# Optimization experiments

Measured on AMD Instinct MI355X. Metric: run time of the kernel, lower is better.

Reference implementation:

```python
import jax, jax.numpy as jnp
import numpy as np

B, T, C, H = 8, 1024, 1024, 16
Dh = C // H
EPS = 1e-5


def layernorm(x, g, b):
    m = jnp.mean(x, axis=-1, keepdims=True)
    v = jnp.mean((x - m) ** 2, axis=-1, keepdims=True)
    return g * (x - m) / jnp.sqrt(v + EPS) + b


def setup_inputs() -> dict:
    key = jax.random.key(0)
    ks = jax.random.split(key, 10)
    s = 0.02
    return {
        "x": jax.random.normal(ks[0], (B, T, C), jnp.float32),
        "Wq": jax.random.normal(ks[1], (H, C, Dh), jnp.float32) * s,
        "Wk": jax.random.normal(ks[2], (H, C, Dh), jnp.float32) * s,
        "Wv": jax.random.normal(ks[3], (H, C, Dh), jnp.float32) * s,
        "Wproj": jax.random.normal(ks[4], (C, C), jnp.float32) * s,
        "bproj": jnp.zeros((C,), jnp.float32),
        "W1": jax.random.normal(ks[5], (C, C), jnp.float32) * s,
        "b1": jnp.zeros((C,), jnp.float32),
        "W2": jax.random.normal(ks[6], (C, C), jnp.float32) * s,
        "b2": jnp.zeros((C,), jnp.float32),
        "g1": jnp.ones((C,), jnp.float32),
        "beta1": jnp.zeros((C,), jnp.float32),
        "g2": jnp.ones((C,), jnp.float32),
        "beta2": jnp.zeros((C,), jnp.float32),
    }


def reference(x, Wq, Wk, Wv, Wproj, bproj, W1, b1, W2, b2, g1, beta1, g2, beta2):
    # pre-LN multi-head causal self-attention + residual
    xn = layernorm(x, g1, beta1)
    q = jnp.einsum("btc,hcd->bhtd", xn, Wq)
    k = jnp.einsum("btc,hcd->bhtd", xn, Wk)
    v = jnp.einsum("btc,hcd->bhtd", xn, Wv)
    scores = jnp.einsum("bhtd,bhsd->bhts", q, k) * (Dh ** -0.5)
    causal = jnp.tril(jnp.ones((T, T), bool))  # [T,T]
    scores = jnp.where(causal, scores, -jnp.inf)
    wei = jax.nn.softmax(scores, axis=-1)
    attn = jnp.einsum("bhts,bhsd->bhtd", wei, v)
    attn = attn.transpose(0, 2, 1, 3).reshape(B, T, C)  # concat heads
    x = x + attn @ Wproj + bproj
    # pre-LN MLP (n_emb -> n_emb, ReLU, n_emb -> n_emb) + residual
    xn2 = layernorm(x, g2, beta2)
    h = jax.nn.relu(xn2 @ W1 + b1)
    x = x + h @ W2 + b2
    return x
```

## Files before the change

kernel.cpp:

```cpp
#include <hip/hip_runtime.h>
#include <hip/hip_bf16.h>

#define KDIM 1024

typedef __bf16  bf16x8  __attribute__((ext_vector_type(8)));
typedef float   floatx4 __attribute__((ext_vector_type(4)));

__device__ inline short f2bf(float f) {
    unsigned u = __float_as_uint(f);
    u += 0x7fffu + ((u >> 16) & 1u);
    return (short)(u >> 16);
}
__device__ inline float bf2f(short s) {
    return __uint_as_float(((unsigned)(unsigned short)s) << 16);
}

__device__ inline floatx4 mfma16(bf16x8 a, bf16x8 b, floatx4 c) {
    return __builtin_amdgcn_mfma_f32_16x16x32_bf16(a, b, c, 0, 0, 0);
}

__device__ inline void load_lds16(const void* g, void* l) {
    __builtin_amdgcn_global_load_lds(
        (__attribute__((address_space(1))) void*)(unsigned long long)g,
        (__attribute__((address_space(3))) void*)(unsigned)(unsigned long long)l,
        16, 0, 0);
}

template <bool BF16IN>
__global__ __launch_bounds__(256) void ln_kernel(
    const void* __restrict__ xv, const float* __restrict__ g,
    const float* __restrict__ be, short* __restrict__ out)
{
    const int row = blockIdx.x, tid = threadIdx.x;
    float4 v;
    if constexpr (BF16IN) {
        const short4 s4 = ((const short4*)xv)[(size_t)row * 256 + tid];
        v.x = bf2f(s4.x); v.y = bf2f(s4.y); v.z = bf2f(s4.z); v.w = bf2f(s4.w);
    } else {
        v = ((const float4*)xv)[(size_t)row * 256 + tid];
    }
    float s  = v.x + v.y + v.z + v.w;
    float s2 = v.x * v.x + v.y * v.y + v.z * v.z + v.w * v.w;
    #pragma unroll
    for (int off = 32; off; off >>= 1) {
        s  += __shfl_down(s, off);
        s2 += __shfl_down(s2, off);
    }
    __shared__ float red1[4], red2[4];
    const int w = tid >> 6, lane = tid & 63;
    if (lane == 0) { red1[w] = s; red2[w] = s2; }
    __syncthreads();
    s  = red1[0] + red1[1] + red1[2] + red1[3];
    s2 = red2[0] + red2[1] + red2[2] + red2[3];
    const float mean = s * (1.0f / 1024.0f);
    const float var  = s2 * (1.0f / 1024.0f) - mean * mean;
    const float rstd = rsqrtf(var + 1e-5f);
    const float4 gg = ((const float4*)g)[tid];
    const float4 bb = ((const float4*)be)[tid];
    short4 o;
    o.x = f2bf((v.x - mean) * rstd * gg.x + bb.x);
    o.y = f2bf((v.y - mean) * rstd * gg.y + bb.y);
    o.z = f2bf((v.z - mean) * rstd * gg.z + bb.z);
    o.w = f2bf((v.w - mean) * rstd * gg.w + bb.w);
    *(short4*)(out + (size_t)row * 1024 + tid * 4) = o;
}

__global__ void pack_all(const float* __restrict__ Wq, const float* __restrict__ Wk,
                         const float* __restrict__ Wv, const float* __restrict__ Wproj,
                         const float* __restrict__ W1, const float* __restrict__ W2,
                         short* __restrict__ qkvT, short* __restrict__ projT,
                         short* __restrict__ w1T, short* __restrict__ w2T)
{
    __shared__ float tile[32][33];
    const int bx = blockIdx.x, c0 = blockIdx.y * 32;
    const int tx = threadIdx.x, ty = threadIdx.y;
    if (bx < 96) {
        const int n0 = bx * 32;
        const int grp = n0 >> 10;
        const float* W = (grp == 0) ? Wq : (grp == 1 ? Wk : Wv);
        const int nb = n0 & 1023, hh = nb >> 6, d0 = nb & 63;
        #pragma unroll
        for (int j = 0; j < 32; j += 8)
            tile[ty + j][tx] = W[hh * 65536 + (c0 + ty + j) * 64 + d0 + tx];
        __syncthreads();
        #pragma unroll
        for (int j = 0; j < 32; j += 8)
            qkvT[(size_t)(n0 + ty + j) * 1024 + c0 + tx] = f2bf(tile[tx][ty + j]);
    } else {
        const int which = (bx - 96) >> 5;
        const int n0 = ((bx - 96) & 31) * 32;
        const float* src = (which == 0) ? Wproj : (which == 1 ? W1 : W2);
        short* dst = (which == 0) ? projT : (which == 1 ? w1T : w2T);
        #pragma unroll
        for (int j = 0; j < 32; j += 8)
            tile[ty + j][tx] = src[(size_t)(c0 + ty + j) * 1024 + n0 + tx];
        __syncthreads();
        #pragma unroll
        for (int j = 0; j < 32; j += 8)
            dst[(size_t)(n0 + ty + j) * 1024 + c0 + tx] = f2bf(tile[tx][ty + j]);
    }
}

template <int EPI, bool SWAP, int TM>
__global__ __launch_bounds__(256, 4) void gemm_bt(
    const short* __restrict__ A, const short* __restrict__ BT, int N,
    const float* __restrict__ bias, const float* __restrict__ residF,
    const short* __restrict__ residH,
    float* __restrict__ outF, short* __restrict__ outH,
    short* __restrict__ qO, short* __restrict__ kO, short* __restrict__ vtO)
{
    constexpr int IT = TM / 32;
    constexpr int PP = (8192 / TM) / 8;
    const int tid = threadIdx.x, lane = tid & 63, w = tid >> 6;
    const int wm = w >> 1, wn = w & 1;
    const int mi = lane & 15, quad = lane >> 4;
    const int lid = blockIdx.x + gridDim.x * blockIdx.y;
    const int xcd = lid & 7, i8 = lid >> 3;
    const int rowBase = (xcd * PP + (i8 % PP)) * TM;
    const int colBase = (i8 / PP) * 128;

    __shared__ alignas(16) short As[2][TM * 32];
    __shared__ alignas(16) short Bs[2][128 * 32];

    const floatx4 z4 = {0.f, 0.f, 0.f, 0.f};
    floatx4 acc[IT][4];
    #pragma unroll
    for (int i = 0; i < IT; ++i)
        #pragma unroll
        for (int j = 0; j < 4; ++j) acc[i][j] = z4;

    auto stage = [&](int k0, int buf) {
        #pragma unroll
        for (int i = 0; i < TM / 64; ++i) {
            const int cb = i * 256 + w * 64;
            const int chunk = cb + lane;
            const int r = chunk >> 2, cc = chunk & 3;
            const int csw = cc ^ ((r >> 1) & 3);
            load_lds16(A + (size_t)(rowBase + r) * KDIM + k0 + csw * 8,
                       (char*)As[buf] + cb * 16);
        }
        #pragma unroll
        for (int i = 0; i < 2; ++i) {
            const int cb = i * 256 + w * 64;
            const int chunk = cb + lane;
            const int r = chunk >> 2, cc = chunk & 3;
            const int csw = cc ^ ((r >> 1) & 3);
            load_lds16(BT + (size_t)(colBase + r) * KDIM + k0 + csw * 8,
                       (char*)Bs[buf] + cb * 16);
        }
    };

    auto compute = [&](const short* Ac, const short* Bc) {
        bf16x8 af[IT], bfv[4];
        #pragma unroll
        for (int it = 0; it < IT; ++it) {
            const int ra = wm * (TM / 2) + it * 16 + mi;
            af[it] = *(const bf16x8*)(Ac + ra * 32 + ((quad ^ ((ra >> 1) & 3)) << 3));
        }
        #pragma unroll
        for (int jt = 0; jt < 4; ++jt) {
            const int rb = wn * 64 + jt * 16 + mi;
            bfv[jt] = *(const bf16x8*)(Bc + rb * 32 + ((quad ^ ((rb >> 1) & 3)) << 3));
        }
        #pragma unroll
        for (int it = 0; it < IT; ++it)
            #pragma unroll
            for (int jt = 0; jt < 4; ++jt) {
                if constexpr (SWAP)
                    acc[it][jt] = mfma16(bfv[jt], af[it], acc[it][jt]);
                else
                    acc[it][jt] = mfma16(af[it], bfv[jt], acc[it][jt]);
            }
    };

    stage(0, 0);
    #pragma unroll 1
    for (int c = 0; c < KDIM / 32; c += 2) {
        __syncthreads();
        if (c + 1 < KDIM / 32) stage((c + 1) * 32, 1);
        compute(As[0], Bs[0]);
        __syncthreads();
        if (c + 2 < KDIM / 32) stage((c + 2) * 32, 0);
        compute(As[1], Bs[1]);
    }

    if constexpr (SWAP) {
        #pragma unroll
        for (int it = 0; it < IT; ++it) {
            const int row = rowBase + wm * (TM / 2) + it * 16 + mi;
            #pragma unroll
            for (int jt = 0; jt < 4; ++jt) {
                const int col0 = colBase + wn * 64 + jt * 16 + quad * 4;
                const floatx4 a4 = acc[it][jt];
                if constexpr (EPI == 0) {
                    if (colBase < 1024) {
                        short4 o;
                        o.x = f2bf(a4[0] * 0.125f); o.y = f2bf(a4[1] * 0.125f);
                        o.z = f2bf(a4[2] * 0.125f); o.w = f2bf(a4[3] * 0.125f);
                        *(short4*)(qO + (size_t)row * 1024 + col0) = o;
                    } else {
                        short4 o;
                        o.x = f2bf(a4[0]); o.y = f2bf(a4[1]);
                        o.z = f2bf(a4[2]); o.w = f2bf(a4[3]);
                        *(short4*)(kO + (size_t)row * 1024 + (col0 - 1024)) = o;
                    }
                } else if constexpr (EPI == 2) {
                    const float4 b4 = *(const float4*)(bias + col0);
                    short4 o;
                    o.x = f2bf(fmaxf(a4[0] + b4.x, 0.f));
                    o.y = f2bf(fmaxf(a4[1] + b4.y, 0.f));
                    o.z = f2bf(fmaxf(a4[2] + b4.z, 0.f));
                    o.w = f2bf(fmaxf(a4[3] + b4.w, 0.f));
                    *(short4*)(outH + (size_t)row * N + col0) = o;
                } else if constexpr (EPI == 4) {
                    const float4 b4 = *(const float4*)(bias + col0);
                    const float4 r4 = *(const float4*)(residF + (size_t)row * N + col0);
                    short4 o;
                    o.x = f2bf(a4[0] + b4.x + r4.x);
                    o.y = f2bf(a4[1] + b4.y + r4.y);
                    o.z = f2bf(a4[2] + b4.z + r4.z);
                    o.w = f2bf(a4[3] + b4.w + r4.w);
                    *(short4*)(outH + (size_t)row * N + col0) = o;
                } else {
                    const float4 b4 = *(const float4*)(bias + col0);
                    const short4 r4 = *(const short4*)(residH + (size_t)row * N + col0);
                    float4 o;
                    o.x = a4[0] + b4.x + bf2f(r4.x);
                    o.y = a4[1] + b4.y + bf2f(r4.y);
                    o.z = a4[2] + b4.z + bf2f(r4.z);
                    o.w = a4[3] + b4.w + bf2f(r4.w);
                    *(float4*)(outF + (size_t)row * N + col0) = o;
                }
            }
        }
    } else {
        #pragma unroll
        for (int it = 0; it < IT; ++it) {
            const int row0 = rowBase + wm * (TM / 2) + it * 16 + quad * 4;
            const int bb = row0 >> 10, t0 = row0 & 1023;
            #pragma unroll
            for (int jt = 0; jt < 4; ++jt) {
                const int c = colBase + wn * 64 + jt * 16 + mi;
                const floatx4 a4 = acc[it][jt];
                short4 o;
                o.x = f2bf(a4[0]); o.y = f2bf(a4[1]);
                o.z = f2bf(a4[2]); o.w = f2bf(a4[3]);
                *(short4*)(vtO + ((size_t)bb << 20) + ((size_t)c << 10) + t0) = o;
            }
        }
    }
}

#define PSTR 88
__device__ __forceinline__ void attn_qk_pv(
    const bf16x8 qf0, const bf16x8 qf1,
    floatx4 (&o)[4], float (&lsum)[4],
    const short* Ks, const short* Vs, short* myP,
    const int mi, const int quad, const int kq, const int diagRowOff)
{
    const floatx4 z4 = {0.f, 0.f, 0.f, 0.f};
    const bool diag = diagRowOff >= 0;
    floatx4 sa[4];
    #pragma unroll
    for (int j = 0; j < 4; ++j) {
        const int row = j * 16 + mi;
        const int sw = row & 7;
        floatx4 s4 = z4;
        s4 = mfma16(qf0, *(const bf16x8*)(Ks + row * 64 + ((quad ^ sw) << 3)), s4);
        s4 = mfma16(qf1, *(const bf16x8*)(Ks + row * 64 + (((quad + 4) ^ sw) << 3)), s4);
        sa[j] = s4;
    }
    #pragma unroll
    for (int j = 0; j < 4; ++j)
        #pragma unroll
        for (int r = 0; r < 4; ++r) {
            float p = __expf(sa[j][r]);
            if (diag && (j * 16 + mi > diagRowOff + quad * 4 + r)) p = 0.f;
            lsum[r] += p;
            myP[(quad * 4 + r) * PSTR + j * 16 + mi] = f2bf(p);
        }
    __asm__ volatile("s_waitcnt lgkmcnt(0)" ::: "memory");
    const bf16x8 pf0 = *(const bf16x8*)(myP + mi * PSTR + kq);
    const bf16x8 pf1 = *(const bf16x8*)(myP + mi * PSTR + 32 + kq);
    #pragma unroll
    for (int d = 0; d < 4; ++d) {
        const int row = d * 16 + mi;
        const int sw = row & 7;
        o[d] = mfma16(pf0, *(const bf16x8*)(Vs + row * 64 + ((quad ^ sw) << 3)), o[d]);
        o[d] = mfma16(pf1, *(const bf16x8*)(Vs + row * 64 + (((quad + 4) ^ sw) << 3)), o[d]);
    }
}

__global__ __launch_bounds__(256, 4) void flash_attn(
    const short* __restrict__ Q, const short* __restrict__ K,
    const short* __restrict__ Vt, short* __restrict__ O)
{
    const int tid = threadIdx.x, lane = tid & 63, w = tid >> 6;
    const int mi = lane & 15, quad = lane >> 4, kq = quad * 8;
    const int lid = blockIdx.x;
    const int xcd = lid & 7, i8 = lid >> 3;
    const int bh = xcd * 16 + (i8 & 15);
    const int pi = i8 >> 4;
    const int h = bh & 15, b = bh >> 4;
    const int tA = pi, tB = 15 - pi;
    const int qbA = tA * 64, qbB = tB * 64;

    __shared__ alignas(16) short Ks[64 * 64];
    __shared__ alignas(16) short Vs[64 * 64];
    __shared__ alignas(16) short Ps[4][16 * PSTR];

    const size_t qoffA = ((size_t)(b * 1024 + qbA + w * 16 + mi)) * 1024 + h * 64;
    const size_t qoffB = ((size_t)(b * 1024 + qbB + w * 16 + mi)) * 1024 + h * 64;
    const bf16x8 qA0 = *(const bf16x8*)(Q + qoffA + kq);
    const bf16x8 qA1 = *(const bf16x8*)(Q + qoffA + 32 + kq);
    const bf16x8 qB0 = *(const bf16x8*)(Q + qoffB + kq);
    const bf16x8 qB1 = *(const bf16x8*)(Q + qoffB + 32 + kq);

    const floatx4 z4 = {0.f, 0.f, 0.f, 0.f};
    floatx4 oA[4], oB[4];
    float lA[4], lB[4];
    #pragma unroll
    for (int i = 0; i < 4; ++i) { oA[i] = z4; oB[i] = z4; lA[i] = 0.f; lB[i] = 0.f; }

    short* myP = &Ps[w][0];
    for (int t = 0; t <= tB; ++t) {
        const int s0 = t * 64;
        __syncthreads();
        #pragma unroll
        for (int i = 0; i < 2; ++i) {
            const int cb = i * 256 + w * 64;
            const int chunk = cb + lane;
            const int r = chunk >> 3, c = chunk & 7;
            const int csw = c ^ (r & 7);
            load_lds16(K + ((size_t)(b * 1024 + s0 + r)) * 1024 + h * 64 + csw * 8,
                       (char*)Ks + cb * 16);
            load_lds16(Vt + ((size_t)b << 20) + ((size_t)(h * 64 + r) << 10) + s0 + csw * 8,
                       (char*)Vs + cb * 16);
        }
        __syncthreads();

        if (t <= tA)
            attn_qk_pv(qA0, qA1, oA, lA, Ks, Vs, myP, mi, quad, kq,
                       (t == tA) ? (w * 16) : -1);
        attn_qk_pv(qB0, qB1, oB, lB, Ks, Vs, myP, mi, quad, kq,
                   (t == tB) ? (w * 16) : -1);
    }

    #pragma unroll
    for (int r = 0; r < 4; ++r) {
        float sA = lA[r], sB = lB[r];
        #pragma unroll
        for (int off = 1; off < 16; off <<= 1) {
            sA += __shfl_xor(sA, off);
            sB += __shfl_xor(sB, off);
        }
        lA[r] = 1.0f / sA;
        lB[r] = 1.0f / sB;
    }
    #pragma unroll
    for (int d = 0; d < 4; ++d)
        #pragma unroll
        for (int r = 0; r < 4; ++r) {
            const int col = h * 64 + d * 16 + mi;
            const int rowA = b * 1024 + qbA + w * 16 + quad * 4 + r;
            const int rowB = b * 1024 + qbB + w * 16 + quad * 4 + r;
            O[(size_t)rowA * 1024 + col] = f2bf(oA[d][r] * lA[r]);
            O[(size_t)rowB * 1024 + col] = f2bf(oB[d][r] * lB[r]);
        }
}

extern "C" void kernel_launch(void* const* d_in, const int* in_sizes, int n_in,
                              void* d_out, int out_size, void* d_ws, size_t ws_size,
                              hipStream_t stream)
{
    (void)in_sizes; (void)n_in; (void)out_size; (void)ws_size;
    const float* x     = (const float*)d_in[0];
    const float* Wq    = (const float*)d_in[1];
    const float* Wk    = (const float*)d_in[2];
    const float* Wv    = (const float*)d_in[3];
    const float* Wproj = (const float*)d_in[4];
    const float* bproj = (const float*)d_in[5];
    const float* W1    = (const float*)d_in[6];
    const float* b1    = (const float*)d_in[7];
    const float* W2    = (const float*)d_in[8];
    const float* b2    = (const float*)d_in[9];
    const float* g1    = (const float*)d_in[10];
    const float* be1   = (const float*)d_in[11];
    const float* g2    = (const float*)d_in[12];
    const float* be2   = (const float*)d_in[13];
    float* out = (float*)d_out;

    char* ws = (char*)d_ws;
    const size_t MB = 1u << 20;
    short* Qb     = (short*)(ws + 0 * MB);
    short* Kb     = (short*)(ws + 16 * MB);
    short* Vtb    = (short*)(ws + 32 * MB);
    short* XN     = (short*)(ws + 48 * MB);
    short* AT     = (short*)(ws + 64 * MB);
    short* R2b    = (short*)(ws + 80 * MB);
    short* WqkvT  = (short*)(ws + 112 * MB);
    short* WprojT = (short*)(ws + 118 * MB);
    short* W1T    = (short*)(ws + 120 * MB);
    short* W2T    = (short*)(ws + 122 * MB);

    pack_all<<<dim3(192, 32), dim3(32, 8), 0, stream>>>(
        Wq, Wk, Wv, Wproj, W1, W2, WqkvT, WprojT, W1T, W2T);

    ln_kernel<false><<<8192, 256, 0, stream>>>(x, g1, be1, XN);

    gemm_bt<0, true, 128><<<dim3(16, 64), 256, 0, stream>>>(XN, WqkvT, 1024,
        nullptr, nullptr, nullptr, nullptr, nullptr, Qb, Kb, nullptr);
    gemm_bt<3, false, 64><<<dim3(8, 128), 256, 0, stream>>>(XN, WqkvT + 2048 * KDIM, 1024,
        nullptr, nullptr, nullptr, nullptr, nullptr, nullptr, nullptr, Vtb);

    flash_attn<<<1024, 256, 0, stream>>>(Qb, Kb, Vtb, AT);

    gemm_bt<4, true, 64><<<dim3(8, 128), 256, 0, stream>>>(AT, WprojT, 1024,
        bproj, x, nullptr, nullptr, R2b, nullptr, nullptr, nullptr);

    ln_kernel<true><<<8192, 256, 0, stream>>>(R2b, g2, be2, XN);

    gemm_bt<2, true, 64><<<dim3(8, 128), 256, 0, stream>>>(XN, W1T, 1024,
        b1, nullptr, nullptr, nullptr, AT, nullptr, nullptr, nullptr);

    gemm_bt<5, true, 64><<<dim3(8, 128), 256, 0, stream>>>(AT, W2T, 1024,
        b2, nullptr, R2b, out, nullptr, nullptr, nullptr, nullptr);
}
```

Baseline: 337.4 us.

## Use 128x128 GEMM tiles everywhere, packed bf16 converts, and exp2 softmax

All GEMMs now use a single 128x128 tile shape, which halves the block count for the N=1024 GEMMs and raises per-block data reuse. Scalar bf16 rounding is replaced with packed float2-to-bf16 conversion in the LayerNorm and GEMM epilogues. The Q scale now folds in log2(e), so attention can use the hardware v_exp_f32 (exp2) directly instead of __expf. With fewer blocks the smaller GEMMs may fill the CUs less completely, and larger tiles use more registers.

Result: faster. 314.8 us (-6.7%).

```diff
diff --git a/kernel.cpp b/kernel.cpp
--- a/kernel.cpp
+++ b/kernel.cpp
@@ -13,6 +13,15 @@
 }
 __device__ inline float bf2f(short s) {
     return __uint_as_float(((unsigned)(unsigned short)s) << 16);
+}
+__device__ inline unsigned pk2bf(float x, float y) {
+    __hip_bfloat162 h = __float22bfloat162_rn(make_float2(x, y));
+    return *reinterpret_cast<unsigned*>(&h);
+}
+__device__ inline float exp2_hw(float x) {
+    float r;
+    __asm__("v_exp_f32 %0, %1" : "=v"(r) : "v"(x));
+    return r;
 }
 
 __device__ inline floatx4 mfma16(bf16x8 a, bf16x8 b, floatx4 c) {
@@ -57,12 +66,11 @@
     const float rstd = rsqrtf(var + 1e-5f);
     const float4 gg = ((const float4*)g)[tid];
     const float4 bb = ((const float4*)be)[tid];
-    short4 o;
-    o.x = f2bf((v.x - mean) * rstd * gg.x + bb.x);
-    o.y = f2bf((v.y - mean) * rstd * gg.y + bb.y);
-    o.z = f2bf((v.z - mean) * rstd * gg.z + bb.z);
-    o.w = f2bf((v.w - mean) * rstd * gg.w + bb.w);
-    *(short4*)(out + (size_t)row * 1024 + tid * 4) = o;
+    const unsigned o01 = pk2bf((v.x - mean) * rstd * gg.x + bb.x,
+                               (v.y - mean) * rstd * gg.y + bb.y);
+    const unsigned o23 = pk2bf((v.z - mean) * rstd * gg.z + bb.z,
+                               (v.w - mean) * rstd * gg.w + bb.w);
+    *(uint2*)(out + (size_t)row * 1024 + tid * 4) = make_uint2(o01, o23);
 }
 
 __global__ void pack_all(const float* __restrict__ Wq, const float* __restrict__ Wk,
@@ -101,7 +109,7 @@
     }
 }
 
-template <int EPI, bool SWAP, int TM>
+template <int EPI, bool SWAP>
 __global__ __launch_bounds__(256, 4) void gemm_bt(
     const short* __restrict__ A, const short* __restrict__ BT, int N,
     const float* __restrict__ bias, const float* __restrict__ residF,
@@ -109,52 +117,43 @@
     float* __restrict__ outF, short* __restrict__ outH,
     short* __restrict__ qO, short* __restrict__ kO, short* __restrict__ vtO)
 {
-    constexpr int IT = TM / 32;
-    constexpr int PP = (8192 / TM) / 8;
     const int tid = threadIdx.x, lane = tid & 63, w = tid >> 6;
     const int wm = w >> 1, wn = w & 1;
     const int mi = lane & 15, quad = lane >> 4;
     const int lid = blockIdx.x + gridDim.x * blockIdx.y;
     const int xcd = lid & 7, i8 = lid >> 3;
-    const int rowBase = (xcd * PP + (i8 % PP)) * TM;
-    const int colBase = (i8 / PP) * 128;
-
-    __shared__ alignas(16) short As[2][TM * 32];
+    const int rowBase = (xcd * 8 + (i8 & 7)) * 128;
+    const int colBase = (i8 >> 3) * 128;
+
+    __shared__ alignas(16) short As[2][128 * 32];
     __shared__ alignas(16) short Bs[2][128 * 32];
 
     const floatx4 z4 = {0.f, 0.f, 0.f, 0.f};
-    floatx4 acc[IT][4];
-    #pragma unroll
-    for (int i = 0; i < IT; ++i)
+    floatx4 acc[4][4];
+    #pragma unroll
+    for (int i = 0; i < 4; ++i)
         #pragma unroll
         for (int j = 0; j < 4; ++j) acc[i][j] = z4;
 
     auto stage = [&](int k0, int buf) {
         #pragma unroll
-        for (int i = 0; i < TM / 64; ++i) {
+        for (int i = 0; i < 2; ++i) {
             const int cb = i * 256 + w * 64;
             const int chunk = cb + lane;
             const int r = chunk >> 2, cc = chunk & 3;
             const int csw = cc ^ ((r >> 1) & 3);
             load_lds16(A + (size_t)(rowBase + r) * KDIM + k0 + csw * 8,
                        (char*)As[buf] + cb * 16);
-        }
-        #pragma unroll
-        for (int i = 0; i < 2; ++i) {
-            const int cb = i * 256 + w * 64;
-            const int chunk = cb + lane;
-            const int r = chunk >> 2, cc = chunk & 3;
-            const int csw = cc ^ ((r >> 1) & 3);
             load_lds16(BT + (size_t)(colBase + r) * KDIM + k0 + csw * 8,
                        (char*)Bs[buf] + cb * 16);
         }
     };
 
     auto compute = [&](const short* Ac, const short* Bc) {
-        bf16x8 af[IT], bfv[4];
-        #pragma unroll
-        for (int it = 0; it < IT; ++it) {
-            const int ra = wm * (TM / 2) + it * 16 + mi;
+        bf16x8 af[4], bfv[4];
+        #pragma unroll
+        for (int it = 0; it < 4; ++it) {
+            const int ra = wm * 64 + it * 16 + mi;
             af[it] = *(const bf16x8*)(Ac + ra * 32 + ((quad ^ ((ra >> 1) & 3)) << 3));
         }
         #pragma unroll
@@ -163,7 +162,7 @@
             bfv[jt] = *(const bf16x8*)(Bc + rb * 32 + ((quad ^ ((rb >> 1) & 3)) << 3));
         }
         #pragma unroll
-        for (int it = 0; it < IT; ++it)
+        for (int it = 0; it < 4; ++it)
             #pragma unroll
             for (int jt = 0; jt < 4; ++jt) {
                 if constexpr (SWAP)
@@ -186,41 +185,33 @@
 
     if constexpr (SWAP) {
         #pragma unroll
-        for (int it = 0; it < IT; ++it) {
-            const int row = rowBase + wm * (TM / 2) + it * 16 + mi;
+        for (int it = 0; it < 4; ++it) {
+            const int row = rowBase + wm * 64 + it * 16 + mi;
             #pragma unroll
             for (int jt = 0; jt < 4; ++jt) {
                 const int col0 = colBase + wn * 64 + jt * 16 + quad * 4;
                 const floatx4 a4 = acc[it][jt];
                 if constexpr (EPI == 0) {
                     if (colBase < 1024) {
-                        short4 o;
-                        o.x = f2bf(a4[0] * 0.125f); o.y = f2bf(a4[1] * 0.125f);
-                        o.z = f2bf(a4[2] * 0.125f); o.w = f2bf(a4[3] * 0.125f);
-                        *(short4*)(qO + (size_t)row * 1024 + col0) = o;
+                        const float qs = 0.18033688011112042f;
+                        *(uint2*)(qO + (size_t)row * 1024 + col0) =
+                            make_uint2(pk2bf(a4[0] * qs, a4[1] * qs),
+                                       pk2bf(a4[2] * qs, a4[3] * qs));
                     } else {
-                        short4 o;
-                        o.x = f2bf(a4[0]); o.y = f2bf(a4[1]);
-                        o.z = f2bf(a4[2]); o.w = f2bf(a4[3]);
-                        *(short4*)(kO + (size_t)row * 1024 + (col0 - 1024)) = o;
+                        *(uint2*)(kO + (size_t)row * 1024 + (col0 - 1024)) =
+                            make_uint2(pk2bf(a4[0], a4[1]), pk2bf(a4[2], a4[3]));
                     }
                 } else if constexpr (EPI == 2) {
                     const float4 b4 = *(const float4*)(bias + col0);
-                    short4 o;
-                    o.x = f2bf(fmaxf(a4[0] + b4.x, 0.f));
-                    o.y = f2bf(fmaxf(a4[1] + b4.y, 0.f));
-                    o.z = f2bf(fmaxf(a4[2] + b4.z, 0.f));
-                    o.w = f2bf(fmaxf(a4[3] + b4.w, 0.f));
-                    *(short4*)(outH + (size_t)row * N + col0) = o;
+                    *(uint2*)(outH + (size_t)row * N + col0) =
+                        make_uint2(pk2bf(fmaxf(a4[0] + b4.x, 0.f), fmaxf(a4[1] + b4.y, 0.f)),
+                                   pk2bf(fmaxf(a4[2] + b4.z, 0.f), fmaxf(a4[3] + b4.w, 0.f)));
                 } else if constexpr (EPI == 4) {
                     const float4 b4 = *(const float4*)(bias + col0);
                     const float4 r4 = *(const float4*)(residF + (size_t)row * N + col0);
-                    short4 o;
-                    o.x = f2bf(a4[0] + b4.x + r4.x);
-                    o.y = f2bf(a4[1] + b4.y + r4.y);
-                    o.z = f2bf(a4[2] + b4.z + r4.z);
-                    o.w = f2bf(a4[3] + b4.w + r4.w);
-                    *(short4*)(outH + (size_t)row * N + col0) = o;
+                    *(uint2*)(outH + (size_t)row * N + col0) =
+                        make_uint2(pk2bf(a4[0] + b4.x + r4.x, a4[1] + b4.y + r4.y),
+                                   pk2bf(a4[2] + b4.z + r4.z, a4[3] + b4.w + r4.w));
                 } else {
                     const float4 b4 = *(const float4*)(bias + col0);
                     const short4 r4 = *(const short4*)(residH + (size_t)row * N + col0);
@@ -235,17 +226,15 @@
         }
     } else {
         #pragma unroll
-        for (int it = 0; it < IT; ++it) {
-            const int row0 = rowBase + wm * (TM / 2) + it * 16 + quad * 4;
+        for (int it = 0; it < 4; ++it) {
+            const int row0 = rowBase + wm * 64 + it * 16 + quad * 4;
             const int bb = row0 >> 10, t0 = row0 & 1023;
             #pragma unroll
             for (int jt = 0; jt < 4; ++jt) {
                 const int c = colBase + wn * 64 + jt * 16 + mi;
                 const floatx4 a4 = acc[it][jt];
-                short4 o;
-                o.x = f2bf(a4[0]); o.y = f2bf(a4[1]);
-                o.z = f2bf(a4[2]); o.w = f2bf(a4[3]);
-                *(short4*)(vtO + ((size_t)bb << 20) + ((size_t)c << 10) + t0) = o;
+                *(uint2*)(vtO + ((size_t)bb << 20) + ((size_t)c << 10) + t0) =
+                    make_uint2(pk2bf(a4[0], a4[1]), pk2bf(a4[2], a4[3]));
             }
         }
     }
@@ -271,14 +260,21 @@
         sa[j] = s4;
     }
     #pragma unroll
-    for (int j = 0; j < 4; ++j)
+    for (int j = 0; j < 4; ++j) {
+        float p[4];
         #pragma unroll
         for (int r = 0; r < 4; ++r) {
-            float p = __expf(sa[j][r]);
-            if (diag && (j * 16 + mi > diagRowOff + quad * 4 + r)) p = 0.f;
-            lsum[r] += p;
-            myP[(quad * 4 + r) * PSTR + j * 16 + mi] = f2bf(p);
-        }
+            p[r] = exp2_hw(sa[j][r]);
+            if (diag && (j * 16 + mi > diagRowOff + quad * 4 + r)) p[r] = 0.f;
+            lsum[r] += p[r];
+        }
+        const unsigned ua = pk2bf(p[0], p[1]);
+        const unsigned ub = pk2bf(p[2], p[3]);
+        myP[(quad * 4 + 0) * PSTR + j * 16 + mi] = (short)ua;
+        myP[(quad * 4 + 1) * PSTR + j * 16 + mi] = (short)(ua >> 16);
+        myP[(quad * 4 + 2) * PSTR + j * 16 + mi] = (short)ub;
+        myP[(quad * 4 + 3) * PSTR + j * 16 + mi] = (short)(ub >> 16);
+    }
     __asm__ volatile("s_waitcnt lgkmcnt(0)" ::: "memory");
     const bf16x8 pf0 = *(const bf16x8*)(myP + mi * PSTR + kq);
     const bf16x8 pf1 = *(const bf16x8*)(myP + mi * PSTR + 32 + kq);
@@ -408,21 +404,21 @@
 
     ln_kernel<false><<<8192, 256, 0, stream>>>(x, g1, be1, XN);
 
-    gemm_bt<0, true, 128><<<dim3(16, 64), 256, 0, stream>>>(XN, WqkvT, 1024,
+    gemm_bt<0, true><<<dim3(16, 64), 256, 0, stream>>>(XN, WqkvT, 1024,
         nullptr, nullptr, nullptr, nullptr, nullptr, Qb, Kb, nullptr);
-    gemm_bt<3, false, 64><<<dim3(8, 128), 256, 0, stream>>>(XN, WqkvT + 2048 * KDIM, 1024,
+    gemm_bt<3, false><<<dim3(8, 64), 256, 0, stream>>>(XN, WqkvT + 2048 * KDIM, 1024,
         nullptr, nullptr, nullptr, nullptr, nullptr, nullptr, nullptr, Vtb);
 
     flash_attn<<<1024, 256, 0, stream>>>(Qb, Kb, Vtb, AT);
 
-    gemm_bt<4, true, 64><<<dim3(8, 128), 256, 0, stream>>>(AT, WprojT, 1024,
+    gemm_bt<4, true><<<dim3(8, 64), 256, 0, stream>>>(AT, WprojT, 1024,
         bproj, x, nullptr, nullptr, R2b, nullptr, nullptr, nullptr);
 
     ln_kernel<true><<<8192, 256, 0, stream>>>(R2b, g2, be2, XN);
 
-    gemm_bt<2, true, 64><<<dim3(8, 128), 256, 0, stream>>>(XN, W1T, 1024,
+    gemm_bt<2, true><<<dim3(8, 64), 256, 0, stream>>>(XN, W1T, 1024,
         b1, nullptr, nullptr, nullptr, AT, nullptr, nullptr, nullptr);
 
-    gemm_bt<5, true, 64><<<dim3(8, 128), 256, 0, stream>>>(AT, W2T, 1024,
+    gemm_bt<5, true><<<dim3(8, 64), 256, 0, stream>>>(AT, W2T, 1024,
         b2, nullptr, R2b, out, nullptr, nullptr, nullptr, nullptr);
 }
```
